# Performance work log

Measured on AMD Instinct MI355X. Metric: run time of the kernel, lower is better.

## Reference

```python
import jax, jax.numpy as jnp
import numpy as np

N, M, C = 200000, 32, 9
VX, VY = 0.2, 0.2
X_OFF, Y_OFF = 0.1, -39.9  # vx/2 + pc_range[0], vy/2 + pc_range[1]
EPS = 1e-3
UNITS = 16  # 64 // 4 per branch

SPATIO_IDX = np.array([0, 1, 2, 5, 6, 7, 8, 9])
VEL_IDX = np.array([3, 10])
SNR_IDX = np.array([4, 11])
LOGIT_IDX = np.array([12, 13, 14, 15])  # num_classes == 3


def setup_inputs() -> dict:
    key = jax.random.key(0)
    ks = jax.random.split(key, 10)
    features = jax.random.normal(ks[0], (N, M, C), jnp.float32)
    num_points = jax.random.randint(ks[1], (N,), 1, M + 1, jnp.int32)
    coors = jnp.concatenate([
        jnp.zeros((N, 2), jnp.int32),
        jax.random.randint(ks[2], (N, 1), 0, 400, jnp.int32),  # y index
        jax.random.randint(ks[3], (N, 1), 0, 352, jnp.int32),  # x index
    ], axis=1)
    w1 = jax.random.normal(ks[4], (UNITS, 8), jnp.float32) * 0.2
    w2 = jax.random.normal(ks[5], (UNITS, 2), jnp.float32) * 0.2
    w3 = jax.random.normal(ks[6], (UNITS, 2), jnp.float32) * 0.2
    w4 = jax.random.normal(ks[7], (UNITS, 4), jnp.float32) * 0.2
    gamma = 1.0 + 0.1 * jax.random.normal(ks[8], (4, UNITS), jnp.float32)
    beta = 0.1 * jax.random.normal(ks[9], (4, UNITS), jnp.float32)
    return {"features": features, "w1": w1, "w2": w2, "w3": w3, "w4": w4,
            "gamma": gamma, "beta": beta, "num_points": num_points, "coors": coors}


def _branch(x, w, g, b):
    # tiny linear (no bias) + BN1d in training mode (stats over N and M)
    y = jnp.einsum('nmc,uc->nmu', x, w)
    mu = y.mean(axis=(0, 1))
    var = y.var(axis=(0, 1))  # biased, matching torch BN normalization
    return (y - mu) * jax.lax.rsqrt(var + EPS) * g + b


def reference(features, w1, w2, w3, w4, gamma, beta, num_points, coors):
    dtype = features.dtype
    npf = num_points.astype(dtype)[:, None, None]  # (N,1,1)

    xyz = features[:, :, :3]
    f_cluster = xyz - xyz.sum(axis=1, keepdims=True) / npf  # (N,M,3)

    cx = coors[:, 3].astype(dtype)[:, None] * VX + X_OFF
    cy = coors[:, 2].astype(dtype)[:, None] * VY + Y_OFF
    f_center = jnp.stack([features[:, :, 0] - cx,
                          features[:, :, 1] - cy], axis=-1)  # (N,M,2)

    vs = features[:, :, 3:5]
    vs_center = vs - vs.sum(axis=1, keepdims=True) / npf  # (N,M,2)

    # legacy=True: f_center aliases features[:, :, :2], so raw cols 0,1 get overwritten
    raw_mod = jnp.concatenate([f_center, features[:, :, 2:]], axis=-1)  # (N,M,9)
    feat = jnp.concatenate([raw_mod, f_cluster, f_center, vs_center], axis=-1)  # (N,M,16)

    mask = (jnp.arange(M)[None, :] < num_points[:, None]).astype(dtype)[:, :, None]
    feat = feat * mask

    x = jnp.concatenate([
        _branch(feat[:, :, SPATIO_IDX], w1, gamma[0], beta[0]),
        _branch(feat[:, :, VEL_IDX],    w2, gamma[1], beta[1]),
        _branch(feat[:, :, SNR_IDX],    w3, gamma[2], beta[2]),
        _branch(feat[:, :, LOGIT_IDX],  w4, gamma[3], beta[3]),
    ], axis=-1)  # (N,M,64)
    x = jax.nn.relu(x)
    return x.max(axis=1)  # max over points, then squeeze of (N,1,64) -> (N,64)
```

## Files before the change

### kernel.cpp

```cpp
#include <hip/hip_runtime.h>
#include <math.h>
#include <stdint.h>


typedef unsigned short u16_t;
typedef __bf16 bf16x8 __attribute__((ext_vector_type(8)));
typedef __bf16 bf16x2_t __attribute__((ext_vector_type(2)));
typedef float floatx16 __attribute__((ext_vector_type(16)));

#define N_P     200000
#define NCHUNK  25000
#define CNT_TOT 6400000.0

__device__ __forceinline__ float bf2f(u16_t u) {
  return __builtin_bit_cast(float, ((unsigned)u) << 16);
}
__device__ __forceinline__ u16_t f2bf(float f) {
  unsigned u = __builtin_bit_cast(unsigned, f);
  u += 0x7FFFu + ((u >> 16) & 1u);
  return (u16_t)(u >> 16);
}
__device__ __forceinline__ unsigned packbf(float a, float b) {
  bf16x2_t v; v[0] = (__bf16)a; v[1] = (__bf16)b;
  return __builtin_bit_cast(unsigned, v);
}
__device__ __forceinline__ float h2lo(unsigned u) {
  return (float)__builtin_bit_cast(_Float16, (unsigned short)(u & 0xFFFFu));
}
__device__ __forceinline__ float h2hi(unsigned u) {
  return (float)__builtin_bit_cast(_Float16, (unsigned short)(u >> 16));
}

template<bool BF16>
__device__ __forceinline__ float ldval(const void* p, size_t i) {
  if constexpr (BF16) return bf2f(((const u16_t*)p)[i]);
  else                return ((const float*)p)[i];
}

struct Pairs { int pi[52]; int pj[52]; int pa[52]; int pb[52]; };
constexpr Pairs makePairs() {
  Pairs P{};
  int n = 0;
  const int L0[8] = {0, 1, 2, 5, 6, 7, 8, 9};
  for (int a = 0; a < 8; ++a)
    for (int b = a; b < 8; ++b) { P.pi[n]=L0[a]; P.pj[n]=L0[b]; P.pa[n]=a; P.pb[n]=b; ++n; }
  const int L1[2] = {3, 10};
  for (int a = 0; a < 2; ++a)
    for (int b = a; b < 2; ++b) { P.pi[n]=L1[a]; P.pj[n]=L1[b]; P.pa[n]=a; P.pb[n]=b; ++n; }
  const int L2[2] = {4, 11};
  for (int a = 0; a < 2; ++a)
    for (int b = a; b < 2; ++b) { P.pi[n]=L2[a]; P.pj[n]=L2[b]; P.pa[n]=a; P.pb[n]=b; ++n; }
  const int L3[4] = {12, 13, 14, 15};
  for (int a = 0; a < 4; ++a)
    for (int b = a; b < 4; ++b) { P.pi[n]=L3[a]; P.pj[n]=L3[b]; P.pa[n]=a; P.pb[n]=b; ++n; }
  return P;
}
constexpr Pairs PT = makePairs();

__global__ void k_detect(const u16_t* __restrict__ f, int* __restrict__ flag) {
  int tid = threadIdx.x;
  int cnt = 0;
  for (int i = 0; i < 4; ++i) {
    unsigned v = f[(size_t)(tid * 4 + i) * 2];
    unsigned e = (v >> 7) & 0xFF;
    cnt += (e >= 100 && e <= 140) ? 1 : 0;
  }
  for (int s = 1; s < 64; s <<= 1) cnt += __shfl_xor(cnt, s);
  if (tid == 0) *flag = (cnt >= 160) ? 1 : 0;
}

template<bool BF16>
__device__ __forceinline__ void derive_feat(
    const void* __restrict__ feats, const int* __restrict__ nump,
    const int* __restrict__ coors, int p, int m, float* feat) {
  size_t base = ((size_t)p * 32 + m) * 9;
  float r[9];
  if constexpr (BF16) {
#pragma unroll
    for (int c = 0; c < 9; ++c) r[c] = bf2f(((const u16_t*)feats)[base + c]);
  } else {
    const float* fp = (const float*)feats + base;
    float v0[4], v1[4];
    __builtin_memcpy(v0, fp, 16);
    __builtin_memcpy(v1, fp + 4, 16);
    r[0]=v0[0]; r[1]=v0[1]; r[2]=v0[2]; r[3]=v0[3];
    r[4]=v1[0]; r[5]=v1[1]; r[6]=v1[2]; r[7]=v1[3];
    r[8]=fp[8];
  }
  float sx = r[0], sy = r[1], sz = r[2], svx = r[3], svy = r[4];
#pragma unroll
  for (int sft = 1; sft < 32; sft <<= 1) {
    sx  += __shfl_xor(sx,  sft);
    sy  += __shfl_xor(sy,  sft);
    sz  += __shfl_xor(sz,  sft);
    svx += __shfl_xor(svx, sft);
    svy += __shfl_xor(svy, sft);
  }
  int np = nump[p];
  float inv = 1.0f / (float)np;
  float cx = (float)coors[p * 4 + 3] * 0.2f + 0.1f;
  float cy = (float)coors[p * 4 + 2] * 0.2f - 39.9f;
  feat[0] = r[0] - cx;
  feat[1] = r[1] - cy;
  feat[2] = r[2]; feat[3] = r[3]; feat[4] = r[4];
  feat[5] = r[5]; feat[6] = r[6]; feat[7] = r[7]; feat[8] = r[8];
  feat[9]  = r[0] - sx * inv;
  feat[10] = r[1] - sy * inv;
  feat[11] = r[2] - sz * inv;
  feat[12] = feat[0];
  feat[13] = feat[1];
  feat[14] = r[3] - svx * inv;
  feat[15] = r[4] - svy * inv;
  if (m >= np) {
#pragma unroll
    for (int c = 0; c < 16; ++c) feat[c] = 0.0f;
  }
}

template<bool BF16>
__device__ __forceinline__ float wval(int u, int c,
    const void* w1, const void* w2, const void* w3, const void* w4) {
  int b = u >> 4, k = u & 15;
  if (b == 0) {
    int k2 = (c <= 2) ? c : ((c >= 5 && c <= 9) ? c - 2 : -1);
    return (k2 >= 0) ? ldval<BF16>(w1, k * 8 + k2) : 0.0f;
  } else if (b == 1) {
    if (c == 3)  return ldval<BF16>(w2, k * 2 + 0);
    if (c == 10) return ldval<BF16>(w2, k * 2 + 1);
    return 0.0f;
  } else if (b == 2) {
    if (c == 4)  return ldval<BF16>(w3, k * 2 + 0);
    if (c == 11) return ldval<BF16>(w3, k * 2 + 1);
    return 0.0f;
  }
  if (c >= 12) return ldval<BF16>(w4, k * 4 + (c - 12));
  return 0.0f;
}

template<bool BF16>
__device__ __forceinline__ void pack_frags(int u,
    const void* w1, const void* w2, const void* w3, const void* w4,
    const void* gamma,
    uint4* wsB0hi, uint4* wsB0lo, uint4* wsB1hi, uint4* wsB1lo) {
  int n = u & 31;
  float g0 = ldval<BF16>(gamma, n);
  float g1 = ldval<BF16>(gamma, n + 32);
  float sg0 = (g0 < 0.0f) ? -1.0f : 1.0f;
  float sg1 = (g1 < 0.0f) ? -1.0f : 1.0f;
  u16_t h0[8], l0[8], h1[8], l1[8];
#pragma unroll
  for (int j = 0; j < 8; ++j) {
    int c = ((u >> 5) << 3) + j;
    float v0 = wval<BF16>(n,      c, w1, w2, w3, w4) * sg0;
    float v1 = wval<BF16>(n + 32, c, w1, w2, w3, w4) * sg1;
    h0[j] = f2bf(v0); h1[j] = f2bf(v1);
    l0[j] = BF16 ? (u16_t)0 : f2bf(v0 - bf2f(h0[j]));
    l1[j] = BF16 ? (u16_t)0 : f2bf(v1 - bf2f(h1[j]));
  }
  uint4 a0, a1, c0, c1;
  a0.x = h0[0] | ((unsigned)h0[1] << 16); a0.y = h0[2] | ((unsigned)h0[3] << 16);
  a0.z = h0[4] | ((unsigned)h0[5] << 16); a0.w = h0[6] | ((unsigned)h0[7] << 16);
  c0.x = l0[0] | ((unsigned)l0[1] << 16); c0.y = l0[2] | ((unsigned)l0[3] << 16);
  c0.z = l0[4] | ((unsigned)l0[5] << 16); c0.w = l0[6] | ((unsigned)l0[7] << 16);
  a1.x = h1[0] | ((unsigned)h1[1] << 16); a1.y = h1[2] | ((unsigned)h1[3] << 16);
  a1.z = h1[4] | ((unsigned)h1[5] << 16); a1.w = h1[6] | ((unsigned)h1[7] << 16);
  c1.x = l1[0] | ((unsigned)l1[1] << 16); c1.y = l1[2] | ((unsigned)l1[3] << 16);
  c1.z = l1[4] | ((unsigned)l1[5] << 16); c1.w = l1[6] | ((unsigned)l1[7] << 16);
  wsB0hi[u] = a0; wsB0lo[u] = c0;
  wsB1hi[u] = a1; wsB1lo[u] = c1;
}


template<bool BF16>
__global__ void k_prep(const void* __restrict__ w1, const void* __restrict__ w2,
                       const void* __restrict__ w3, const void* __restrict__ w4,
                       const void* __restrict__ gamma,
                       const int* __restrict__ flag,
                       uint4* __restrict__ wsB0hi, uint4* __restrict__ wsB0lo,
                       uint4* __restrict__ wsB1hi, uint4* __restrict__ wsB1lo) {
  if (*flag != (BF16 ? 1 : 0)) return;
  pack_frags<BF16>(threadIdx.x, w1, w2, w3, w4, gamma,
                   wsB0hi, wsB0lo, wsB1hi, wsB1lo);
}

template<bool BF16>
__global__ __launch_bounds__(256, 4) void k_fused(
    const void* __restrict__ feats, const int* __restrict__ nump,
    const int* __restrict__ coors, const int* __restrict__ flag,
    const uint4* __restrict__ wsB0hi, const uint4* __restrict__ wsB0lo,
    const uint4* __restrict__ wsB1hi, const uint4* __restrict__ wsB1lo,
    u16_t* __restrict__ mm, float* __restrict__ part, int g1) {
  if (*flag != (BF16 ? 1 : 0)) return;
  __shared__ float red[4][128];
  int tid = threadIdx.x;
  int wave = tid >> 6, lane = tid & 63;
  int pp = (lane >> 5) & 1, m = lane & 31;
  bool lo = (lane < 32);

  bf16x8 B0h = __builtin_bit_cast(bf16x8, wsB0hi[lane]);
  bf16x8 B1h = __builtin_bit_cast(bf16x8, wsB1hi[lane]);
  bf16x8 B0l, B1l;
  if constexpr (!BF16) {
    B0l = __builtin_bit_cast(bf16x8, wsB0lo[lane]);
    B1l = __builtin_bit_cast(bf16x8, wsB1lo[lane]);
  }
  floatx16 z;
#pragma unroll
  for (int i = 0; i < 16; ++i) z[i] = 0.0f;

  float sA0 = 0.0f, sQ0 = 0.0f, sA1 = 0.0f, sQ1 = 0.0f;

  for (int chunk = blockIdx.x; chunk < NCHUNK; chunk += g1) {
    int p = chunk * 8 + wave * 2 + pp;
    float feat[16];
    derive_feat<BF16>(feats, nump, coors, p, m, feat);

    unsigned H[8], L[8];
#pragma unroll
    for (int j = 0; j < 8; ++j) {
      float a0 = feat[2 * j], a1 = feat[2 * j + 1];
      __bf16 h0 = (__bf16)a0, h1 = (__bf16)a1;
      bf16x2_t hv; hv[0] = h0; hv[1] = h1;
      H[j] = __builtin_bit_cast(unsigned, hv);
      if constexpr (!BF16) {
        L[j] = packbf(a0 - (float)h0, a1 - (float)h1);
      }
    }
    unsigned Q0[4], Q1[4], Q0l[4], Q1l[4];
#pragma unroll
    for (int j = 0; j < 4; ++j) {
      unsigned pre = lo ? H[4 + j] : H[j];
      unsigned t = (unsigned)__shfl_xor((int)pre, 32);
      Q0[j] = lo ? H[j] : t;
      Q1[j] = lo ? t : H[4 + j];
      if constexpr (!BF16) {
        unsigned prel = lo ? L[4 + j] : L[j];
        unsigned tl = (unsigned)__shfl_xor((int)prel, 32);
        Q0l[j] = lo ? L[j] : tl;
        Q1l[j] = lo ? tl : L[4 + j];
      }
    }

#pragma unroll
    for (int q = 0; q < 2; ++q) {
      uint4 ah;
      if (q == 0) { ah.x = Q0[0]; ah.y = Q0[1]; ah.z = Q0[2]; ah.w = Q0[3]; }
      else        { ah.x = Q1[0]; ah.y = Q1[1]; ah.z = Q1[2]; ah.w = Q1[3]; }
      bf16x8 Ah = __builtin_bit_cast(bf16x8, ah);
      floatx16 d0, d1;
      if constexpr (BF16) {
        d0 = __builtin_amdgcn_mfma_f32_32x32x16_bf16(Ah, B0h, z, 0, 0, 0);
        d1 = __builtin_amdgcn_mfma_f32_32x32x16_bf16(Ah, B1h, z, 0, 0, 0);
      } else {
        uint4 al;
        if (q == 0) { al.x = Q0l[0]; al.y = Q0l[1]; al.z = Q0l[2]; al.w = Q0l[3]; }
        else        { al.x = Q1l[0]; al.y = Q1l[1]; al.z = Q1l[2]; al.w = Q1l[3]; }
        bf16x8 Al = __builtin_bit_cast(bf16x8, al);
        d0 = __builtin_amdgcn_mfma_f32_32x32x16_bf16(Al, B0h, z, 0, 0, 0);
        d0 = __builtin_amdgcn_mfma_f32_32x32x16_bf16(Ah, B0l, d0, 0, 0, 0);
        d0 = __builtin_amdgcn_mfma_f32_32x32x16_bf16(Ah, B0h, d0, 0, 0, 0);
        d1 = __builtin_amdgcn_mfma_f32_32x32x16_bf16(Al, B1h, z, 0, 0, 0);
        d1 = __builtin_amdgcn_mfma_f32_32x32x16_bf16(Ah, B1l, d1, 0, 0, 0);
        d1 = __builtin_amdgcn_mfma_f32_32x32x16_bf16(Ah, B1h, d1, 0, 0, 0);
      }
      float mx0 = d0[0], mx1 = d1[0];
      float l0s = d0[0], l1s = d1[0];
      float l0q = d0[0] * d0[0], l1q = d1[0] * d1[0];
#pragma unroll
      for (int r = 1; r < 15; r += 2) {
        float a = d0[r], a2 = d0[r + 1], b = d1[r], b2 = d1[r + 1];
        mx0 = fmaxf(fmaxf(mx0, a), a2);
        mx1 = fmaxf(fmaxf(mx1, b), b2);
        l0s += a + a2;  l1s += b + b2;
        l0q = fmaf(a, a, l0q);  l0q = fmaf(a2, a2, l0q);
        l1q = fmaf(b, b, l1q);  l1q = fmaf(b2, b2, l1q);
      }
      {
        float a = d0[15], b = d1[15];
        mx0 = fmaxf(mx0, a); mx1 = fmaxf(mx1, b);
        l0s += a; l1s += b;
        l0q = fmaf(a, a, l0q); l1q = fmaf(b, b, l1q);
      }
      sA0 += l0s; sQ0 += l0q; sA1 += l1s; sQ1 += l1q;
      mx0 = fmaxf(mx0, __shfl_xor(mx0, 32));
      mx1 = fmaxf(mx1, __shfl_xor(mx1, 32));
      float val = lo ? mx0 : mx1;
      _Float16 hf = (_Float16)val;
      int pq = chunk * 8 + wave * 2 + q;
      mm[(size_t)pq * 64 + lane] = __builtin_bit_cast(u16_t, hf);
    }
  }

  sA0 += __shfl_xor(sA0, 32); sQ0 += __shfl_xor(sQ0, 32);
  sA1 += __shfl_xor(sA1, 32); sQ1 += __shfl_xor(sQ1, 32);
  if (lane < 32) {
    red[wave][lane]      = sA0;
    red[wave][32 + lane] = sA1;
    red[wave][64 + lane] = sQ0;
    red[wave][96 + lane] = sQ1;
  }
  __syncthreads();
  if (tid < 128)
    part[(size_t)tid * g1 + blockIdx.x] =
        red[0][tid] + red[1][tid] + red[2][tid] + red[3][tid];
}

__global__ void k_reduce2(const float* __restrict__ part,
                          double* __restrict__ mom, int g1) {
  int j = blockIdx.x, tid = threadIdx.x;
  double s = 0.0;
  for (int b = tid; b < g1; b += 256) s += (double)part[(size_t)j * g1 + b];
  __shared__ double red[256];
  red[tid] = s;
  __syncthreads();
  for (int off = 128; off; off >>= 1) {
    if (tid < off) red[tid] += red[tid + off];
    __syncthreads();
  }
  if (tid == 0) mom[j] = red[0];
}

template<bool BF16>
__global__ void k_fin2(const double* __restrict__ mom,
                       const void* __restrict__ gamma, const void* __restrict__ beta,
                       const int* __restrict__ flag,
                       float* __restrict__ wsS, float* __restrict__ wsT) {
  if (*flag != (BF16 ? 1 : 0)) return;
  int u = threadIdx.x;
  double mu  = mom[u] / CNT_TOT;
  double var = mom[64 + u] / CNT_TOT - mu * mu;
  float g  = ldval<BF16>(gamma, u);
  float be = ldval<BF16>(beta, u);
  float S = (float)(1.0 / sqrt(var + 1e-3)) * fabsf(g);
  float T = be - (float)mu * S;
  wsS[u] = S;
  wsT[u] = T;
}

template<bool BF16>
__global__ __launch_bounds__(256) void k_out(
    const uint4* __restrict__ mm4, const float* __restrict__ wsS,
    const float* __restrict__ wsT, const int* __restrict__ flag,
    void* __restrict__ outv) {
  if (*flag != (BF16 ? 1 : 0)) return;
  __shared__ float sS[64], sT[64];
  int tid = threadIdx.x;
  if (tid < 64) { sS[tid] = wsS[tid]; sT[tid] = wsT[tid]; }
  __syncthreads();
  const int total = N_P * 8;
  for (int i = blockIdx.x * 256 + tid; i < total; i += gridDim.x * 256) {
    uint4 v = mm4[i];
    unsigned w[4] = {v.x, v.y, v.z, v.w};
    int u0 = (i & 7) * 8;
    float o[8];
#pragma unroll
    for (int j = 0; j < 4; ++j) {
      float mxa = h2lo(w[j]), mxb = h2hi(w[j]);
      o[2 * j]     = fmaxf(fmaf(sS[u0 + 2 * j],     mxa, sT[u0 + 2 * j]),     0.0f);
      o[2 * j + 1] = fmaxf(fmaf(sS[u0 + 2 * j + 1], mxb, sT[u0 + 2 * j + 1]), 0.0f);
    }
    if constexpr (BF16) {
      uint4 r;
      r.x = packbf(o[0], o[1]); r.y = packbf(o[2], o[3]);
      r.z = packbf(o[4], o[5]); r.w = packbf(o[6], o[7]);
      ((uint4*)outv)[i] = r;
    } else {
      float4 f0, f1;
      f0.x = o[0]; f0.y = o[1]; f0.z = o[2]; f0.w = o[3];
      f1.x = o[4]; f1.y = o[5]; f1.z = o[6]; f1.w = o[7];
      ((float4*)outv)[i * 2]     = f0;
      ((float4*)outv)[i * 2 + 1] = f1;
    }
  }
}


template<bool BF16>
__global__ void k_moments(const void* __restrict__ feats,
                          const int* __restrict__ nump,
                          const int* __restrict__ coors,
                          const int* __restrict__ flag,
                          float* __restrict__ part, int g1) {
  if (*flag != (BF16 ? 1 : 0)) return;
  int tid = threadIdx.x;
  int wave = tid >> 6, lane = tid & 63;
  int pp = (lane >> 5) & 1, m = lane & 31;
  float acc[68];
#pragma unroll
  for (int i = 0; i < 68; ++i) acc[i] = 0.0f;

  for (int chunk = blockIdx.x; chunk < NCHUNK; chunk += g1) {
    int p = chunk * 8 + wave * 2 + pp;
    float feat[16];
    derive_feat<BF16>(feats, nump, coors, p, m, feat);
#pragma unroll
    for (int c = 0; c < 16; ++c) acc[c] += feat[c];
#pragma unroll
    for (int t = 0; t < 52; ++t)
      acc[16 + t] = fmaf(feat[PT.pi[t]], feat[PT.pj[t]], acc[16 + t]);
  }

#pragma unroll
  for (int k = 0; k < 68; ++k) {
    float v = acc[k];
#pragma unroll
    for (int sft = 1; sft < 64; sft <<= 1) v += __shfl_xor(v, sft);
    acc[k] = v;
  }
  __shared__ float red[4][68];
  if (lane == 0) {
#pragma unroll
    for (int k = 0; k < 68; ++k) red[wave][k] = acc[k];
  }
  __syncthreads();
  if (tid < 68) {
    float t = red[0][tid] + red[1][tid] + red[2][tid] + red[3][tid];
    part[(size_t)tid * g1 + blockIdx.x] = t;
  }
}

__global__ void k_reduce(const float* __restrict__ part,
                         float* __restrict__ mom, int g1) {
  int j = blockIdx.x, tid = threadIdx.x;
  float s = 0.0f;
  for (int b = tid; b < g1; b += 256) s += part[(size_t)j * g1 + b];
  __shared__ float red[256];
  red[tid] = s;
  __syncthreads();
  for (int off = 128; off; off >>= 1) {
    if (tid < off) red[tid] += red[tid + off];
    __syncthreads();
  }
  if (tid == 0) mom[j] = red[0];
}

template<bool BF16>
__global__ void k_finalize(const float* __restrict__ mom,
    const void* __restrict__ w1, const void* __restrict__ w2,
    const void* __restrict__ w3, const void* __restrict__ w4,
    const void* __restrict__ gamma, const void* __restrict__ beta,
    const int* __restrict__ flag,
    float* __restrict__ wsS, float* __restrict__ wsT,
    uint4* __restrict__ wsB0hi, uint4* __restrict__ wsB0lo,
    uint4* __restrict__ wsB1hi, uint4* __restrict__ wsB1lo) {
  if (*flag != (BF16 ? 1 : 0)) return;
  int u = threadIdx.x;
  const int CHOFF[4] = {0, 8, 10, 12};
  const int CCNT[4]  = {8, 2, 2, 4};
  const int LCH[16]  = {0,1,2,5,6,7,8,9, 3,10, 4,11, 12,13,14,15};
  const int PBASE[4] = {0, 36, 39, 42};
  const int PCNTB[4] = {36, 3, 3, 10};

  int b = u >> 4, k = u & 15;
  const void* wsrc = (b == 0) ? w1 : (b == 1) ? w2 : (b == 2) ? w3 : w4;
  int cc = CCNT[b];
  float  w[8];
  double mf[8];
  for (int i = 0; i < 8; ++i) { w[i] = 0.0f; mf[i] = 0.0; }
  for (int i = 0; i < cc; ++i) {
    w[i]  = ldval<BF16>(wsrc, k * cc + i);
    mf[i] = (double)mom[LCH[CHOFF[b] + i]] / CNT_TOT;
  }
  double mu = 0.0;
  for (int i = 0; i < cc; ++i) mu += (double)w[i] * mf[i];
  double var = 0.0;
  for (int t = 0; t < PCNTB[b]; ++t) {
    int idx = PBASE[b] + t;
    int a = PT.pa[idx], b2 = PT.pb[idx];
    double e2  = (double)mom[16 + idx] / CNT_TOT;
    double cov = e2 - mf[a] * mf[b2];
    var += ((a == b2) ? 1.0 : 2.0) * (double)w[a] * (double)w[b2] * cov;
  }
  float g  = ldval<BF16>(gamma, u);
  float be = ldval<BF16>(beta, u);
  float S = (float)(1.0 / sqrt(var + 1e-3)) * g;
  float T = be - (float)mu * S;
  wsS[u] = fabsf(S);
  wsT[u] = T;

  pack_frags<BF16>(u, w1, w2, w3, w4, gamma, wsB0hi, wsB0lo, wsB1hi, wsB1lo);
}

template<bool BF16>
__global__ __launch_bounds__(256) void k_main(
    const void* __restrict__ feats, const int* __restrict__ nump,
    const int* __restrict__ coors, const int* __restrict__ flag,
    const float* __restrict__ wsS, const float* __restrict__ wsT,
    const uint4* __restrict__ wsB0hi, const uint4* __restrict__ wsB0lo,
    const uint4* __restrict__ wsB1hi, const uint4* __restrict__ wsB1lo,
    void* __restrict__ outv) {
  if (*flag != (BF16 ? 1 : 0)) return;
  constexpr int TILE = 8 * 32 * 3;
  __shared__ uint4 featL[(BF16 ? 1 : 2) * TILE];
  int tid = threadIdx.x;
  int wave = tid >> 6, lane = tid & 63;
  int pp = (lane >> 5) & 1, m = lane & 31;

  bf16x8 B0h = __builtin_bit_cast(bf16x8, wsB0hi[lane]);
  bf16x8 B1h = __builtin_bit_cast(bf16x8, wsB1hi[lane]);
  bf16x8 B0l, B1l;
  if constexpr (!BF16) {
    B0l = __builtin_bit_cast(bf16x8, wsB0lo[lane]);
    B1l = __builtin_bit_cast(bf16x8, wsB1lo[lane]);
  }
  int ucol = lane & 31;
  float s0 = wsS[ucol],      t0 = wsT[ucol];
  float s1 = wsS[ucol + 32], t1 = wsT[ucol + 32];

  int wp = wave * 2 + pp;
  int p  = blockIdx.x * 8 + wp;
  float feat[16];
  derive_feat<BF16>(feats, nump, coors, p, m, feat);

  unsigned pkh[8], pkl[8];
#pragma unroll
  for (int j = 0; j < 8; ++j) {
    float a0 = feat[2 * j], a1 = feat[2 * j + 1];
    u16_t h0 = f2bf(a0), h1 = f2bf(a1);
    pkh[j] = (unsigned)h0 | ((unsigned)h1 << 16);
    if constexpr (!BF16) {
      u16_t q0 = f2bf(a0 - bf2f(h0)), q1 = f2bf(a1 - bf2f(h1));
      pkl[j] = (unsigned)q0 | ((unsigned)q1 << 16);
    }
  }
  uint4 v;
  v.x = pkh[0]; v.y = pkh[1]; v.z = pkh[2]; v.w = pkh[3];
  featL[(wp * 32 + m) * 3 + 0] = v;
  v.x = pkh[4]; v.y = pkh[5]; v.z = pkh[6]; v.w = pkh[7];
  featL[(wp * 32 + m) * 3 + 1] = v;
  if constexpr (!BF16) {
    v.x = pkl[0]; v.y = pkl[1]; v.z = pkl[2]; v.w = pkl[3];
    featL[TILE + (wp * 32 + m) * 3 + 0] = v;
    v.x = pkl[4]; v.y = pkl[5]; v.z = pkl[6]; v.w = pkl[7];
    featL[TILE + (wp * 32 + m) * 3 + 1] = v;
  }
  __syncthreads();

  floatx16 z;
#pragma unroll
  for (int i = 0; i < 16; ++i) z[i] = 0.0f;

#pragma unroll
  for (int q = 0; q < 2; ++q) {
    int wq = wave * 2 + q;
    int ridx = (wq * 32 + (lane & 31)) * 3 + (lane >> 5);
    bf16x8 Ah = __builtin_bit_cast(bf16x8, featL[ridx]);
    floatx16 d0, d1;
    if constexpr (BF16) {
      d0 = __builtin_amdgcn_mfma_f32_32x32x16_bf16(Ah, B0h, z, 0, 0, 0);
      d1 = __builtin_amdgcn_mfma_f32_32x32x16_bf16(Ah, B1h, z, 0, 0, 0);
    } else {
      bf16x8 Al = __builtin_bit_cast(bf16x8, featL[TILE + ridx]);
      d0 = __builtin_amdgcn_mfma_f32_32x32x16_bf16(Al, B0h, z, 0, 0, 0);
      d0 = __builtin_amdgcn_mfma_f32_32x32x16_bf16(Ah, B0l, d0, 0, 0, 0);
      d0 = __builtin_amdgcn_mfma_f32_32x32x16_bf16(Ah, B0h, d0, 0, 0, 0);
      d1 = __builtin_amdgcn_mfma_f32_32x32x16_bf16(Al, B1h, z, 0, 0, 0);
      d1 = __builtin_amdgcn_mfma_f32_32x32x16_bf16(Ah, B1l, d1, 0, 0, 0);
      d1 = __builtin_amdgcn_mfma_f32_32x32x16_bf16(Ah, B1h, d1, 0, 0, 0);
    }
    float mx0 = fmaf(d0[0], s0, t0);
    float mx1 = fmaf(d1[0], s1, t1);
#pragma unroll
    for (int r = 1; r < 16; ++r) {
      mx0 = fmaxf(mx0, fmaf(d0[r], s0, t0));
      mx1 = fmaxf(mx1, fmaf(d1[r], s1, t1));
    }
    mx0 = fmaxf(mx0, __shfl_xor(mx0, 32));
    mx1 = fmaxf(mx1, __shfl_xor(mx1, 32));
    mx0 = fmaxf(mx0, 0.0f);
    mx1 = fmaxf(mx1, 0.0f);
    float val = (lane < 32) ? mx0 : mx1;
    size_t oidx = (size_t)(blockIdx.x * 8 + wq) * 64 + lane;
    if constexpr (BF16) ((u16_t*)outv)[oidx] = f2bf(val);
    else                ((float*)outv)[oidx] = val;
  }
}

extern "C" void kernel_launch(void* const* d_in, const int* in_sizes, int n_in,
                              void* d_out, int out_size, void* d_ws, size_t ws_size,
                              hipStream_t stream) {
  (void)in_sizes; (void)n_in; (void)out_size;
  const void* feats = d_in[0];
  const void* w1    = d_in[1];
  const void* w2    = d_in[2];
  const void* w3    = d_in[3];
  const void* w4    = d_in[4];
  const void* gamma = d_in[5];
  const void* beta  = d_in[6];
  const int*  nump  = (const int*)d_in[7];
  const int*  coors = (const int*)d_in[8];

  char* ws = (char*)d_ws;
  int*   flag   = (int*)(ws + 0);
  float* wsS    = (float*)(ws + 64);
  float* wsT    = (float*)(ws + 320);
  uint4* wsB0hi = (uint4*)(ws + 576);
  uint4* wsB0lo = (uint4*)(ws + 1600);
  uint4* wsB1hi = (uint4*)(ws + 2624);
  uint4* wsB1lo = (uint4*)(ws + 3648);

  const int g1f = 2048;
  double* mom2  = (double*)(ws + 4672);
  float*  part2 = (float*)(ws + 5696);
  u16_t*  mm    = (u16_t*)(ws + 1054336);
  size_t need_fused = 1054336ull + (size_t)N_P * 64ull * 2ull;

  if (ws_size >= need_fused) {
    k_detect<<<1, 64, 0, stream>>>((const u16_t*)feats, flag);
    k_prep<true ><<<1, 64, 0, stream>>>(w1, w2, w3, w4, gamma, flag,
                                        wsB0hi, wsB0lo, wsB1hi, wsB1lo);
    k_prep<false><<<1, 64, 0, stream>>>(w1, w2, w3, w4, gamma, flag,
                                        wsB0hi, wsB0lo, wsB1hi, wsB1lo);
    k_fused<true ><<<g1f, 256, 0, stream>>>(feats, nump, coors, flag,
                                            wsB0hi, wsB0lo, wsB1hi, wsB1lo, mm, part2, g1f);
    k_fused<false><<<g1f, 256, 0, stream>>>(feats, nump, coors, flag,
                                            wsB0hi, wsB0lo, wsB1hi, wsB1lo, mm, part2, g1f);
    k_reduce2<<<128, 256, 0, stream>>>(part2, mom2, g1f);
    k_fin2<true ><<<1, 64, 0, stream>>>(mom2, gamma, beta, flag, wsS, wsT);
    k_fin2<false><<<1, 64, 0, stream>>>(mom2, gamma, beta, flag, wsS, wsT);
    k_out<true ><<<2048, 256, 0, stream>>>((const uint4*)mm, wsS, wsT, flag, d_out);
    k_out<false><<<2048, 256, 0, stream>>>((const uint4*)mm, wsS, wsT, flag, d_out);
    return;
  }

  float* mom  = (float*)(ws + 4672);
  float* part = (float*)(ws + 5120);

  int g1 = 1024;
  size_t need = 5120 + (size_t)68 * (size_t)g1 * 4;
  if (need > ws_size) {
    size_t avail = (ws_size > 5120) ? (ws_size - 5120) : 0;
    g1 = (int)(avail / (68 * 4));
    if (g1 > 1024) g1 = 1024;
    if (g1 < 8) g1 = 8;
  }

  k_detect<<<1, 64, 0, stream>>>((const u16_t*)feats, flag);
  k_moments<true ><<<g1, 256, 0, stream>>>(feats, nump, coors, flag, part, g1);
  k_moments<false><<<g1, 256, 0, stream>>>(feats, nump, coors, flag, part, g1);
  k_reduce<<<68, 256, 0, stream>>>(part, mom, g1);
  k_finalize<true ><<<1, 64, 0, stream>>>(mom, w1, w2, w3, w4, gamma, beta, flag,
                                          wsS, wsT, wsB0hi, wsB0lo, wsB1hi, wsB1lo);
  k_finalize<false><<<1, 64, 0, stream>>>(mom, w1, w2, w3, w4, gamma, beta, flag,
                                          wsS, wsT, wsB0hi, wsB0lo, wsB1hi, wsB1lo);
  k_main<true ><<<N_P / 8, 256, 0, stream>>>(feats, nump, coors, flag, wsS, wsT,
                                             wsB0hi, wsB0lo, wsB1hi, wsB1lo, d_out);
  k_main<false><<<N_P / 8, 256, 0, stream>>>(feats, nump, coors, flag, wsS, wsT,
                                             wsB0hi, wsB0lo, wsB1hi, wsB1lo, d_out);
}
```

Baseline: 377.9 us.

## Merge dtype-templated launches into runtime dispatch and prefetch two chunks per iteration

```diff
diff --git a/kernel.cpp b/kernel.cpp
--- a/kernel.cpp
+++ b/kernel.cpp
@@ -57,66 +57,6 @@
 }
 constexpr Pairs PT = makePairs();
 
-__global__ void k_detect(const u16_t* __restrict__ f, int* __restrict__ flag) {
-  int tid = threadIdx.x;
-  int cnt = 0;
-  for (int i = 0; i < 4; ++i) {
-    unsigned v = f[(size_t)(tid * 4 + i) * 2];
-    unsigned e = (v >> 7) & 0xFF;
-    cnt += (e >= 100 && e <= 140) ? 1 : 0;
-  }
-  for (int s = 1; s < 64; s <<= 1) cnt += __shfl_xor(cnt, s);
-  if (tid == 0) *flag = (cnt >= 160) ? 1 : 0;
-}
-
-template<bool BF16>
-__device__ __forceinline__ void derive_feat(
-    const void* __restrict__ feats, const int* __restrict__ nump,
-    const int* __restrict__ coors, int p, int m, float* feat) {
-  size_t base = ((size_t)p * 32 + m) * 9;
-  float r[9];
-  if constexpr (BF16) {
-#pragma unroll
-    for (int c = 0; c < 9; ++c) r[c] = bf2f(((const u16_t*)feats)[base + c]);
-  } else {
-    const float* fp = (const float*)feats + base;
-    float v0[4], v1[4];
-    __builtin_memcpy(v0, fp, 16);
-    __builtin_memcpy(v1, fp + 4, 16);
-    r[0]=v0[0]; r[1]=v0[1]; r[2]=v0[2]; r[3]=v0[3];
-    r[4]=v1[0]; r[5]=v1[1]; r[6]=v1[2]; r[7]=v1[3];
-    r[8]=fp[8];
-  }
-  float sx = r[0], sy = r[1], sz = r[2], svx = r[3], svy = r[4];
-#pragma unroll
-  for (int sft = 1; sft < 32; sft <<= 1) {
-    sx  += __shfl_xor(sx,  sft);
-    sy  += __shfl_xor(sy,  sft);
-    sz  += __shfl_xor(sz,  sft);
-    svx += __shfl_xor(svx, sft);
-    svy += __shfl_xor(svy, sft);
-  }
-  int np = nump[p];
-  float inv = 1.0f / (float)np;
-  float cx = (float)coors[p * 4 + 3] * 0.2f + 0.1f;
-  float cy = (float)coors[p * 4 + 2] * 0.2f - 39.9f;
-  feat[0] = r[0] - cx;
-  feat[1] = r[1] - cy;
-  feat[2] = r[2]; feat[3] = r[3]; feat[4] = r[4];
-  feat[5] = r[5]; feat[6] = r[6]; feat[7] = r[7]; feat[8] = r[8];
-  feat[9]  = r[0] - sx * inv;
-  feat[10] = r[1] - sy * inv;
-  feat[11] = r[2] - sz * inv;
-  feat[12] = feat[0];
-  feat[13] = feat[1];
-  feat[14] = r[3] - svx * inv;
-  feat[15] = r[4] - svy * inv;
-  if (m >= np) {
-#pragma unroll
-    for (int c = 0; c < 16; ++c) feat[c] = 0.0f;
-  }
-}
-
 template<bool BF16>
 __device__ __forceinline__ float wval(int u, int c,
     const void* w1, const void* w2, const void* w3, const void* w4) {
@@ -171,26 +111,177 @@
 }
 
 
-template<bool BF16>
-__global__ void k_prep(const void* __restrict__ w1, const void* __restrict__ w2,
+__global__ void k_init(const void* __restrict__ feats,
+                       const void* __restrict__ w1, const void* __restrict__ w2,
                        const void* __restrict__ w3, const void* __restrict__ w4,
                        const void* __restrict__ gamma,
-                       const int* __restrict__ flag,
+                       int* __restrict__ flag,
                        uint4* __restrict__ wsB0hi, uint4* __restrict__ wsB0lo,
                        uint4* __restrict__ wsB1hi, uint4* __restrict__ wsB1lo) {
-  if (*flag != (BF16 ? 1 : 0)) return;
-  pack_frags<BF16>(threadIdx.x, w1, w2, w3, w4, gamma,
-                   wsB0hi, wsB0lo, wsB1hi, wsB1lo);
-}
-
-template<bool BF16>
-__global__ __launch_bounds__(256, 4) void k_fused(
+  const u16_t* f = (const u16_t*)feats;
+  int tid = threadIdx.x;
+  int cnt = 0;
+  for (int i = 0; i < 4; ++i) {
+    unsigned v = f[(size_t)(tid * 4 + i) * 2];
+    unsigned e = (v >> 7) & 0xFF;
+    cnt += (e >= 100 && e <= 140) ? 1 : 0;
+  }
+  for (int s = 1; s < 64; s <<= 1) cnt += __shfl_xor(cnt, s);
+  int bf = (cnt >= 160) ? 1 : 0;
+  if (tid == 0) *flag = bf;
+  if (bf) pack_frags<true >(tid, w1, w2, w3, w4, gamma, wsB0hi, wsB0lo, wsB1hi, wsB1lo);
+  else    pack_frags<false>(tid, w1, w2, w3, w4, gamma, wsB0hi, wsB0lo, wsB1hi, wsB1lo);
+}
+
+struct RawPt {
+  float r[9];
+  float cx, cy;
+  int np;
+};
+
+template<bool BF16>
+__device__ __forceinline__ RawPt load_raw(
     const void* __restrict__ feats, const int* __restrict__ nump,
-    const int* __restrict__ coors, const int* __restrict__ flag,
+    const int* __restrict__ coors, int p, int m) {
+  RawPt o;
+  size_t base = ((size_t)p * 32 + m) * 9;
+  if constexpr (BF16) {
+#pragma unroll
+    for (int c = 0; c < 9; ++c) o.r[c] = bf2f(((const u16_t*)feats)[base + c]);
+  } else {
+    const float* fp = (const float*)feats + base;
+    float v0[4], v1[4];
+    __builtin_memcpy(v0, fp, 16);
+    __builtin_memcpy(v1, fp + 4, 16);
+    o.r[0]=v0[0]; o.r[1]=v0[1]; o.r[2]=v0[2]; o.r[3]=v0[3];
+    o.r[4]=v1[0]; o.r[5]=v1[1]; o.r[6]=v1[2]; o.r[7]=v1[3];
+    o.r[8]=fp[8];
+  }
+  o.np = nump[p];
+  o.cx = (float)coors[p * 4 + 3] * 0.2f + 0.1f;
+  o.cy = (float)coors[p * 4 + 2] * 0.2f - 39.9f;
+  return o;
+}
+
+template<bool BF16>
+__device__ __forceinline__ void process_chunk(
+    const RawPt& R, int chunk, int wave, int lane, int m, bool lo,
+    const bf16x8& B0h, const bf16x8& B1h, const bf16x8& B0l, const bf16x8& B1l,
+    u16_t* __restrict__ mm,
+    float& sA0, float& sQ0, float& sA1, float& sQ1) {
+  float sx = R.r[0], sy = R.r[1], sz = R.r[2], svx = R.r[3], svy = R.r[4];
+#pragma unroll
+  for (int sft = 1; sft < 32; sft <<= 1) {
+    sx  += __shfl_xor(sx,  sft);
+    sy  += __shfl_xor(sy,  sft);
+    sz  += __shfl_xor(sz,  sft);
+    svx += __shfl_xor(svx, sft);
+    svy += __shfl_xor(svy, sft);
+  }
+  float inv = 1.0f / (float)R.np;
+  float feat[16];
+  feat[0] = R.r[0] - R.cx;
+  feat[1] = R.r[1] - R.cy;
+  feat[2] = R.r[2]; feat[3] = R.r[3]; feat[4] = R.r[4];
+  feat[5] = R.r[5]; feat[6] = R.r[6]; feat[7] = R.r[7]; feat[8] = R.r[8];
+  feat[9]  = R.r[0] - sx * inv;
+  feat[10] = R.r[1] - sy * inv;
+  feat[11] = R.r[2] - sz * inv;
+  feat[12] = feat[0];
+  feat[13] = feat[1];
+  feat[14] = R.r[3] - svx * inv;
+  feat[15] = R.r[4] - svy * inv;
+  bool valid = (m < R.np);
+
+  unsigned H[8], L[8];
+#pragma unroll
+  for (int j = 0; j < 8; ++j) {
+    float a0 = feat[2 * j], a1 = feat[2 * j + 1];
+    __bf16 h0 = (__bf16)a0, h1 = (__bf16)a1;
+    bf16x2_t hv; hv[0] = h0; hv[1] = h1;
+    unsigned hw = __builtin_bit_cast(unsigned, hv);
+    H[j] = valid ? hw : 0u;
+    if constexpr (!BF16) {
+      unsigned lw = packbf(a0 - (float)h0, a1 - (float)h1);
+      L[j] = valid ? lw : 0u;
+    }
+  }
+  unsigned Q0[4], Q1[4], Q0l[4], Q1l[4];
+#pragma unroll
+  for (int j = 0; j < 4; ++j) {
+    unsigned pre = lo ? H[4 + j] : H[j];
+    unsigned t = (unsigned)__shfl_xor((int)pre, 32);
+    Q0[j] = lo ? H[j] : t;
+    Q1[j] = lo ? t : H[4 + j];
+    if constexpr (!BF16) {
+      unsigned prel = lo ? L[4 + j] : L[j];
+      unsigned tl = (unsigned)__shfl_xor((int)prel, 32);
+      Q0l[j] = lo ? L[j] : tl;
+      Q1l[j] = lo ? tl : L[4 + j];
+    }
+  }
+
+  floatx16 z;
+#pragma unroll
+  for (int i = 0; i < 16; ++i) z[i] = 0.0f;
+
+#pragma unroll
+  for (int q = 0; q < 2; ++q) {
+    uint4 ah;
+    if (q == 0) { ah.x = Q0[0]; ah.y = Q0[1]; ah.z = Q0[2]; ah.w = Q0[3]; }
+    else        { ah.x = Q1[0]; ah.y = Q1[1]; ah.z = Q1[2]; ah.w = Q1[3]; }
+    bf16x8 Ah = __builtin_bit_cast(bf16x8, ah);
+    floatx16 d0, d1;
+    if constexpr (BF16) {
+      d0 = __builtin_amdgcn_mfma_f32_32x32x16_bf16(Ah, B0h, z, 0, 0, 0);
+      d1 = __builtin_amdgcn_mfma_f32_32x32x16_bf16(Ah, B1h, z, 0, 0, 0);
+    } else {
+      uint4 al;
+      if (q == 0) { al.x = Q0l[0]; al.y = Q0l[1]; al.z = Q0l[2]; al.w = Q0l[3]; }
+      else        { al.x = Q1l[0]; al.y = Q1l[1]; al.z = Q1l[2]; al.w = Q1l[3]; }
+      bf16x8 Al = __builtin_bit_cast(bf16x8, al);
+      d0 = __builtin_amdgcn_mfma_f32_32x32x16_bf16(Al, B0h, z, 0, 0, 0);
+      d0 = __builtin_amdgcn_mfma_f32_32x32x16_bf16(Ah, B0l, d0, 0, 0, 0);
+      d0 = __builtin_amdgcn_mfma_f32_32x32x16_bf16(Ah, B0h, d0, 0, 0, 0);
+      d1 = __builtin_amdgcn_mfma_f32_32x32x16_bf16(Al, B1h, z, 0, 0, 0);
+      d1 = __builtin_amdgcn_mfma_f32_32x32x16_bf16(Ah, B1l, d1, 0, 0, 0);
+      d1 = __builtin_amdgcn_mfma_f32_32x32x16_bf16(Ah, B1h, d1, 0, 0, 0);
+    }
+    float mx0 = d0[0], mx1 = d1[0];
+    float l0s = d0[0], l1s = d1[0];
+    float l0q = d0[0] * d0[0], l1q = d1[0] * d1[0];
+#pragma unroll
+    for (int r = 1; r < 15; r += 2) {
+      float a = d0[r], a2 = d0[r + 1], b = d1[r], b2 = d1[r + 1];
+      mx0 = fmaxf(fmaxf(mx0, a), a2);
+      mx1 = fmaxf(fmaxf(mx1, b), b2);
+      l0s += a + a2;  l1s += b + b2;
+      l0q = fmaf(a, a, l0q);  l0q = fmaf(a2, a2, l0q);
+      l1q = fmaf(b, b, l1q);  l1q = fmaf(b2, b2, l1q);
+    }
+    {
+      float a = d0[15], b = d1[15];
+      mx0 = fmaxf(mx0, a); mx1 = fmaxf(mx1, b);
+      l0s += a; l1s += b;
+      l0q = fmaf(a, a, l0q); l1q = fmaf(b, b, l1q);
+    }
+    sA0 += l0s; sQ0 += l0q; sA1 += l1s; sQ1 += l1q;
+    mx0 = fmaxf(mx0, __shfl_xor(mx0, 32));
+    mx1 = fmaxf(mx1, __shfl_xor(mx1, 32));
+    float val = lo ? mx0 : mx1;
+    _Float16 hf = (_Float16)val;
+    int pq = chunk * 8 + wave * 2 + q;
+    mm[(size_t)pq * 64 + lane] = __builtin_bit_cast(u16_t, hf);
+  }
+}
+
+template<bool BF16>
+__device__ __forceinline__ void fused_body(
+    const void* __restrict__ feats, const int* __restrict__ nump,
+    const int* __restrict__ coors,
     const uint4* __restrict__ wsB0hi, const uint4* __restrict__ wsB0lo,
     const uint4* __restrict__ wsB1hi, const uint4* __restrict__ wsB1lo,
     u16_t* __restrict__ mm, float* __restrict__ part, int g1) {
-  if (*flag != (BF16 ? 1 : 0)) return;
   __shared__ float red[4][128];
   int tid = threadIdx.x;
   int wave = tid >> 6, lane = tid & 63;
@@ -204,91 +295,20 @@
     B0l = __builtin_bit_cast(bf16x8, wsB0lo[lane]);
     B1l = __builtin_bit_cast(bf16x8, wsB1lo[lane]);
   }
-  floatx16 z;
-#pragma unroll
-  for (int i = 0; i < 16; ++i) z[i] = 0.0f;
-
   float sA0 = 0.0f, sQ0 = 0.0f, sA1 = 0.0f, sQ1 = 0.0f;
 
-  for (int chunk = blockIdx.x; chunk < NCHUNK; chunk += g1) {
-    int p = chunk * 8 + wave * 2 + pp;
-    float feat[16];
-    derive_feat<BF16>(feats, nump, coors, p, m, feat);
-
-    unsigned H[8], L[8];
-#pragma unroll
-    for (int j = 0; j < 8; ++j) {
-      float a0 = feat[2 * j], a1 = feat[2 * j + 1];
-      __bf16 h0 = (__bf16)a0, h1 = (__bf16)a1;
-      bf16x2_t hv; hv[0] = h0; hv[1] = h1;
-      H[j] = __builtin_bit_cast(unsigned, hv);
-      if constexpr (!BF16) {
-        L[j] = packbf(a0 - (float)h0, a1 - (float)h1);
-      }
-    }
-    unsigned Q0[4], Q1[4], Q0l[4], Q1l[4];
-#pragma unroll
-    for (int j = 0; j < 4; ++j) {
-      unsigned pre = lo ? H[4 + j] : H[j];
-      unsigned t = (unsigned)__shfl_xor((int)pre, 32);
-      Q0[j] = lo ? H[j] : t;
-      Q1[j] = lo ? t : H[4 + j];
-      if constexpr (!BF16) {
-        unsigned prel = lo ? L[4 + j] : L[j];
-        unsigned tl = (unsigned)__shfl_xor((int)prel, 32);
-        Q0l[j] = lo ? L[j] : tl;
-        Q1l[j] = lo ? tl : L[4 + j];
-      }
-    }
-
-#pragma unroll
-    for (int q = 0; q < 2; ++q) {
-      uint4 ah;
-      if (q == 0) { ah.x = Q0[0]; ah.y = Q0[1]; ah.z = Q0[2]; ah.w = Q0[3]; }
-      else        { ah.x = Q1[0]; ah.y = Q1[1]; ah.z = Q1[2]; ah.w = Q1[3]; }
-      bf16x8 Ah = __builtin_bit_cast(bf16x8, ah);
-      floatx16 d0, d1;
-      if constexpr (BF16) {
-        d0 = __builtin_amdgcn_mfma_f32_32x32x16_bf16(Ah, B0h, z, 0, 0, 0);
-        d1 = __builtin_amdgcn_mfma_f32_32x32x16_bf16(Ah, B1h, z, 0, 0, 0);
-      } else {
-        uint4 al;
-        if (q == 0) { al.x = Q0l[0]; al.y = Q0l[1]; al.z = Q0l[2]; al.w = Q0l[3]; }
-        else        { al.x = Q1l[0]; al.y = Q1l[1]; al.z = Q1l[2]; al.w = Q1l[3]; }
-        bf16x8 Al = __builtin_bit_cast(bf16x8, al);
-        d0 = __builtin_amdgcn_mfma_f32_32x32x16_bf16(Al, B0h, z, 0, 0, 0);
-        d0 = __builtin_amdgcn_mfma_f32_32x32x16_bf16(Ah, B0l, d0, 0, 0, 0);
-        d0 = __builtin_amdgcn_mfma_f32_32x32x16_bf16(Ah, B0h, d0, 0, 0, 0);
-        d1 = __builtin_amdgcn_mfma_f32_32x32x16_bf16(Al, B1h, z, 0, 0, 0);
-        d1 = __builtin_amdgcn_mfma_f32_32x32x16_bf16(Ah, B1l, d1, 0, 0, 0);
-        d1 = __builtin_amdgcn_mfma_f32_32x32x16_bf16(Ah, B1h, d1, 0, 0, 0);
-      }
-      float mx0 = d0[0], mx1 = d1[0];
-      float l0s = d0[0], l1s = d1[0];
-      float l0q = d0[0] * d0[0], l1q = d1[0] * d1[0];
-#pragma unroll
-      for (int r = 1; r < 15; r += 2) {
-        float a = d0[r], a2 = d0[r + 1], b = d1[r], b2 = d1[r + 1];
-        mx0 = fmaxf(fmaxf(mx0, a), a2);
-        mx1 = fmaxf(fmaxf(mx1, b), b2);
-        l0s += a + a2;  l1s += b + b2;
-        l0q = fmaf(a, a, l0q);  l0q = fmaf(a2, a2, l0q);
-        l1q = fmaf(b, b, l1q);  l1q = fmaf(b2, b2, l1q);
-      }
-      {
-        float a = d0[15], b = d1[15];
-        mx0 = fmaxf(mx0, a); mx1 = fmaxf(mx1, b);
-        l0s += a; l1s += b;
-        l0q = fmaf(a, a, l0q); l1q = fmaf(b, b, l1q);
-      }
-      sA0 += l0s; sQ0 += l0q; sA1 += l1s; sQ1 += l1q;
-      mx0 = fmaxf(mx0, __shfl_xor(mx0, 32));
-      mx1 = fmaxf(mx1, __shfl_xor(mx1, 32));
-      float val = lo ? mx0 : mx1;
-      _Float16 hf = (_Float16)val;
-      int pq = chunk * 8 + wave * 2 + q;
-      mm[(size_t)pq * 64 + lane] = __builtin_bit_cast(u16_t, hf);
-    }
+  for (int chunk = blockIdx.x; chunk < NCHUNK; chunk += 2 * g1) {
+    int cB = chunk + g1;
+    bool hasB = (cB < NCHUNK);
+    RawPt ra = load_raw<BF16>(feats, nump, coors, chunk * 8 + wave * 2 + pp, m);
+    RawPt rb;
+    if (hasB)
+      rb = load_raw<BF16>(feats, nump, coors, cB * 8 + wave * 2 + pp, m);
+    process_chunk<BF16>(ra, chunk, wave, lane, m, lo, B0h, B1h, B0l, B1l,
+                        mm, sA0, sQ0, sA1, sQ1);
+    if (hasB)
+      process_chunk<BF16>(rb, cB, wave, lane, m, lo, B0h, B1h, B0l, B1l,
+                          mm, sA0, sQ0, sA1, sQ1);
   }
 
   sA0 += __shfl_xor(sA0, 32); sQ0 += __shfl_xor(sQ0, 32);
@@ -303,6 +323,18 @@
   if (tid < 128)
     part[(size_t)tid * g1 + blockIdx.x] =
         red[0][tid] + red[1][tid] + red[2][tid] + red[3][tid];
+}
+
+__global__ __launch_bounds__(256, 4) void k_fused_all(
+    const void* __restrict__ feats, const int* __restrict__ nump,
+    const int* __restrict__ coors, const int* __restrict__ flag,
+    const uint4* __restrict__ wsB0hi, const uint4* __restrict__ wsB0lo,
+    const uint4* __restrict__ wsB1hi, const uint4* __restrict__ wsB1lo,
+    u16_t* __restrict__ mm, float* __restrict__ part, int g1) {
+  if (*flag)
+    fused_body<true >(feats, nump, coors, wsB0hi, wsB0lo, wsB1hi, wsB1lo, mm, part, g1);
+  else
+    fused_body<false>(feats, nump, coors, wsB0hi, wsB0lo, wsB1hi, wsB1lo, mm, part, g1);
 }
 
 __global__ void k_reduce2(const float* __restrict__ part,
@@ -320,31 +352,30 @@
   if (tid == 0) mom[j] = red[0];
 }
 
-template<bool BF16>
-__global__ void k_fin2(const double* __restrict__ mom,
-                       const void* __restrict__ gamma, const void* __restrict__ beta,
-                       const int* __restrict__ flag,
-                       float* __restrict__ wsS, float* __restrict__ wsT) {
-  if (*flag != (BF16 ? 1 : 0)) return;
+__global__ void k_fin2_all(const double* __restrict__ mom,
+                           const void* __restrict__ gamma,
+                           const void* __restrict__ beta,
+                           const int* __restrict__ flag,
+                           float* __restrict__ wsS, float* __restrict__ wsT) {
   int u = threadIdx.x;
+  int bf = *flag;
   double mu  = mom[u] / CNT_TOT;
   double var = mom[64 + u] / CNT_TOT - mu * mu;
-  float g  = ldval<BF16>(gamma, u);
-  float be = ldval<BF16>(beta, u);
+  float g  = bf ? ldval<true>(gamma, u) : ldval<false>(gamma, u);
+  float be = bf ? ldval<true>(beta,  u) : ldval<false>(beta,  u);
   float S = (float)(1.0 / sqrt(var + 1e-3)) * fabsf(g);
   float T = be - (float)mu * S;
   wsS[u] = S;
   wsT[u] = T;
 }
 
-template<bool BF16>
-__global__ __launch_bounds__(256) void k_out(
+__global__ __launch_bounds__(256) void k_out_all(
     const uint4* __restrict__ mm4, const float* __restrict__ wsS,
     const float* __restrict__ wsT, const int* __restrict__ flag,
     void* __restrict__ outv) {
-  if (*flag != (BF16 ? 1 : 0)) return;
   __shared__ float sS[64], sT[64];
   int tid = threadIdx.x;
+  int bf = *flag;
   if (tid < 64) { sS[tid] = wsS[tid]; sT[tid] = wsT[tid]; }
   __syncthreads();
   const int total = N_P * 8;
@@ -359,7 +390,7 @@
       o[2 * j]     = fmaxf(fmaf(sS[u0 + 2 * j],     mxa, sT[u0 + 2 * j]),     0.0f);
       o[2 * j + 1] = fmaxf(fmaf(sS[u0 + 2 * j + 1], mxb, sT[u0 + 2 * j + 1]), 0.0f);
     }
-    if constexpr (BF16) {
+    if (bf) {
       uint4 r;
       r.x = packbf(o[0], o[1]); r.y = packbf(o[2], o[3]);
       r.z = packbf(o[4], o[5]); r.w = packbf(o[6], o[7]);
@@ -374,6 +405,50 @@
   }
 }
 
+
+__global__ void k_detect(const u16_t* __restrict__ f, int* __restrict__ flag) {
+  int tid = threadIdx.x;
+  int cnt = 0;
+  for (int i = 0; i < 4; ++i) {
+    unsigned v = f[(size_t)(tid * 4 + i) * 2];
+    unsigned e = (v >> 7) & 0xFF;
+    cnt += (e >= 100 && e <= 140) ? 1 : 0;
+  }
+  for (int s = 1; s < 64; s <<= 1) cnt += __shfl_xor(cnt, s);
+  if (tid == 0) *flag = (cnt >= 160) ? 1 : 0;
+}
+
+template<bool BF16>
+__device__ __forceinline__ void derive_feat(
+    const void* __restrict__ feats, const int* __restrict__ nump,
+    const int* __restrict__ coors, int p, int m, float* feat) {
+  RawPt R = load_raw<BF16>(feats, nump, coors, p, m);
+  float sx = R.r[0], sy = R.r[1], sz = R.r[2], svx = R.r[3], svy = R.r[4];
+#pragma unroll
+  for (int sft = 1; sft < 32; sft <<= 1) {
+    sx  += __shfl_xor(sx,  sft);
+    sy  += __shfl_xor(sy,  sft);
+    sz  += __shfl_xor(sz,  sft);
+    svx += __shfl_xor(svx, sft);
+    svy += __shfl_xor(svy, sft);
+  }
+  float inv = 1.0f / (float)R.np;
+  feat[0] = R.r[0] - R.cx;
+  feat[1] = R.r[1] - R.cy;
+  feat[2] = R.r[2]; feat[3] = R.r[3]; feat[4] = R.r[4];
+  feat[5] = R.r[5]; feat[6] = R.r[6]; feat[7] = R.r[7]; feat[8] = R.r[8];
+  feat[9]  = R.r[0] - sx * inv;
+  feat[10] = R.r[1] - sy * inv;
+  feat[11] = R.r[2] - sz * inv;
+  feat[12] = feat[0];
+  feat[13] = feat[1];
+  feat[14] = R.r[3] - svx * inv;
+  feat[15] = R.r[4] - svy * inv;
+  if (m >= R.np) {
+#pragma unroll
+    for (int c = 0; c < 16; ++c) feat[c] = 0.0f;
+  }
+}
 
 template<bool BF16>
 __global__ void k_moments(const void* __restrict__ feats,
@@ -606,20 +681,14 @@
   size_t need_fused = 1054336ull + (size_t)N_P * 64ull * 2ull;
 
   if (ws_size >= need_fused) {
-    k_detect<<<1, 64, 0, stream>>>((const u16_t*)feats, flag);
-    k_prep<true ><<<1, 64, 0, stream>>>(w1, w2, w3, w4, gamma, flag,
-                                        wsB0hi, wsB0lo, wsB1hi, wsB1lo);
-    k_prep<false><<<1, 64, 0, stream>>>(w1, w2, w3, w4, gamma, flag,
-                                        wsB0hi, wsB0lo, wsB1hi, wsB1lo);
-    k_fused<true ><<<g1f, 256, 0, stream>>>(feats, nump, coors, flag,
-                                            wsB0hi, wsB0lo, wsB1hi, wsB1lo, mm, part2, g1f);
-    k_fused<false><<<g1f, 256, 0, stream>>>(feats, nump, coors, flag,
-                                            wsB0hi, wsB0lo, wsB1hi, wsB1lo, mm, part2, g1f);
+    k_init<<<1, 64, 0, stream>>>(feats, w1, w2, w3, w4, gamma, flag,
+                                 wsB0hi, wsB0lo, wsB1hi, wsB1lo);
+    k_fused_all<<<g1f, 256, 0, stream>>>(feats, nump, coors, flag,
+                                         wsB0hi, wsB0lo, wsB1hi, wsB1lo,
+                                         mm, part2, g1f);
     k_reduce2<<<128, 256, 0, stream>>>(part2, mom2, g1f);
-    k_fin2<true ><<<1, 64, 0, stream>>>(mom2, gamma, beta, flag, wsS, wsT);
-    k_fin2<false><<<1, 64, 0, stream>>>(mom2, gamma, beta, flag, wsS, wsT);
-    k_out<true ><<<2048, 256, 0, stream>>>((const uint4*)mm, wsS, wsT, flag, d_out);
-    k_out<false><<<2048, 256, 0, stream>>>((const uint4*)mm, wsS, wsT, flag, d_out);
+    k_fin2_all<<<1, 64, 0, stream>>>(mom2, gamma, beta, flag, wsS, wsT);
+    k_out_all<<<2048, 256, 0, stream>>>((const uint4*)mm, wsS, wsT, flag, d_out);
     return;
   }
 
```

Result: faster. 370.1 us (-2.0%).
